# Kernel tuning notes

Hardware: AMD Instinct MI355X
Metric: run time of the kernel (lower is better)

Reference implementation:

```python
import jax, jax.numpy as jnp
import numpy as np

CHEB_K = 3
EMBED_DIM = 16
N_NODES = 2048
DIM = 64


def setup_inputs() -> dict:
    key = jax.random.key(0)
    k1, k2, k3, k4 = jax.random.split(key, 4)
    B, N, T, D = 16, N_NODES, 12, DIM
    x = jax.random.normal(k1, (B, N, T, D), dtype=jnp.float32)
    node_embeddings = jax.random.normal(k2, (N, EMBED_DIM), dtype=jnp.float32)
    # xavier-uniform-ish init for pools
    wp_bound = float(np.sqrt(6.0 / (EMBED_DIM * CHEB_K * D + D)))
    weights_pool = jax.random.uniform(k3, (EMBED_DIM, CHEB_K, D, D), dtype=jnp.float32,
                                      minval=-wp_bound, maxval=wp_bound)
    bias_pool = jax.random.uniform(k4, (EMBED_DIM, D), dtype=jnp.float32)
    return {"x": x, "node_embeddings": node_embeddings,
            "weights_pool": weights_pool, "bias_pool": bias_pool}


def reference(x, node_embeddings, weights_pool, bias_pool):
    B, N, T, D = x.shape
    cheb_k = weights_pool.shape[1]
    # [B,N,T,D] -> [B*T, N, D]
    xr = jnp.transpose(x, (0, 2, 1, 3)).reshape(B * T, N, D)
    # adaptive adjacency: row-softmax of relu gram matrix  [N,N]
    supports = jax.nn.softmax(jax.nn.relu(node_embeddings @ node_embeddings.T), axis=1)
    # Chebyshev polynomial basis of the adaptive support
    support_set = [jnp.eye(N, dtype=supports.dtype), supports]
    for _ in range(2, cheb_k):
        support_set.append(2.0 * supports @ support_set[-1] - support_set[-2])
    supports_k = jnp.stack(support_set, axis=0)  # [K,N,N]
    # hypernetwork: per-node weights/bias from embeddings
    weights = jnp.einsum('nd,dkio->nkio', node_embeddings, weights_pool)  # [N,K,D,D]
    bias = node_embeddings @ bias_pool  # [N,D]
    # graph conv: gather K-hop aggregates, then per-node grouped GEMM
    x_g = jnp.einsum('knm,bmc->bnkc', supports_k, xr)  # [B*T,N,K,D]
    x_gconv = jnp.einsum('bnki,nkio->bno', x_g, weights) + bias  # [B*T,N,D]
    return jnp.transpose(x_gconv.reshape(B, T, N, D), (0, 2, 1, 3))
```

## Files before the change

kernel.cpp:

```cpp
#include <hip/hip_runtime.h>
#include <hip/hip_bf16.h>

#define N_NODES 2048
#define EMB 16
#define NT 12
#define BT 192
#define C_COLS 12288
#define TD 768
#define BSTRIDE (N_NODES * TD)
#define KDIM 2048

typedef unsigned short u16;
typedef unsigned int u32;
typedef __attribute__((ext_vector_type(8))) __bf16 bf16x8;
typedef __attribute__((ext_vector_type(8))) u16 u16x8;
typedef __attribute__((ext_vector_type(4))) float f32x4;

__device__ __forceinline__ u16 f2bfu(float f) {
    u32 u = __float_as_uint(f);
    return (u16)((u + 0x7FFFu + ((u >> 16) & 1u)) >> 16);
}
__device__ __forceinline__ float bfu2f(u16 h) {
    return __uint_as_float(((u32)h) << 16);
}

__device__ __forceinline__ void gl2lds16(const void* g, void* l) {
    __builtin_amdgcn_global_load_lds(
        (const __attribute__((address_space(1))) u32*)g,
        (__attribute__((address_space(3))) u32*)l, 16, 0, 0);
}

__device__ __forceinline__ int cswz(int col, int row) {
    return (col & ~63) | ((((col >> 3) ^ row) & 7) << 3) | (col & 7);
}

__global__ void supports_kernel(const float* __restrict__ E, u16* __restrict__ Sb)
{
    __shared__ float en[EMB];
    __shared__ float red[256];
    const int n = blockIdx.x;
    const int tid = threadIdx.x;
    if (tid < EMB) en[tid] = E[n * EMB + tid];
    __syncthreads();

    float v[8];
    float mx = 0.0f;
    #pragma unroll
    for (int j = 0; j < 8; ++j) {
        const int m = tid + j * 256;
        const float* em = E + m * EMB;
        float acc = 0.f;
        #pragma unroll
        for (int d = 0; d < EMB; ++d) acc += en[d] * em[d];
        acc = fmaxf(acc, 0.f);
        v[j] = acc;
        mx = fmaxf(mx, acc);
    }
    red[tid] = mx;
    __syncthreads();
    for (int s = 128; s > 0; s >>= 1) {
        if (tid < s) red[tid] = fmaxf(red[tid], red[tid + s]);
        __syncthreads();
    }
    mx = red[0];
    __syncthreads();

    float sum = 0.f;
    #pragma unroll
    for (int j = 0; j < 8; ++j) { v[j] = __expf(v[j] - mx); sum += v[j]; }
    red[tid] = sum;
    __syncthreads();
    for (int s = 128; s > 0; s >>= 1) {
        if (tid < s) red[tid] += red[tid + s];
        __syncthreads();
    }
    const float inv = 1.f / red[0];
    #pragma unroll
    for (int j = 0; j < 8; ++j)
        Sb[(size_t)n * KDIM + tid + j * 256] = f2bfu(v[j] * inv);
}

__global__ void supports2_kernel(const float* __restrict__ E, u16* __restrict__ Sb)
{
    __shared__ float en[EMB];
    __shared__ float red[256];
    const int n = blockIdx.x;
    const int tid = threadIdx.x;
    if (tid < EMB) en[tid] = E[n * EMB + tid];
    __syncthreads();

    float v[8];
    float mx = 0.0f;
    #pragma unroll
    for (int j = 0; j < 8; ++j) {
        const int m = tid + j * 256;
        const float* em = E + m * EMB;
        float acc = 0.f;
        #pragma unroll
        for (int d = 0; d < EMB; ++d) acc += en[d] * em[d];
        acc = fmaxf(acc, 0.f);
        v[j] = acc;
        mx = fmaxf(mx, acc);
    }
    red[tid] = mx;
    __syncthreads();
    for (int s = 128; s > 0; s >>= 1) {
        if (tid < s) red[tid] = fmaxf(red[tid], red[tid + s]);
        __syncthreads();
    }
    mx = red[0];
    __syncthreads();

    float sum = 0.f;
    #pragma unroll
    for (int j = 0; j < 8; ++j) { v[j] = __expf(v[j] - mx); sum += v[j]; }
    red[tid] = sum;
    __syncthreads();
    for (int s = 128; s > 0; s >>= 1) {
        if (tid < s) red[tid] += red[tid + s];
        __syncthreads();
    }
    const float inv = 1.f / red[0];
    #pragma unroll
    for (int j = 0; j < 8; ++j) {
        const int m = tid + j * 256;
        Sb[(size_t)n * KDIM + cswz(m, n)] = f2bfu(v[j] * inv);
    }
}

__global__ void strans_kernel(const u16* __restrict__ Sb, u16* __restrict__ SbT)
{
    __shared__ u16 T[64][65];
    const int tid = threadIdx.x;
    const int n0 = blockIdx.y * 64;
    const int j0 = blockIdx.x * 64;
    const int lc = tid & 63;
    const int rg = tid >> 6;
    #pragma unroll
    for (int j = 0; j < 16; ++j) {
        const int r = j * 4 + rg;
        const u16 vv = Sb[(size_t)(n0 + r) * KDIM + j0 + lc];
        const int jt = ((((lc >> 3) ^ (n0 + r)) & 7) << 3) | (lc & 7);
        T[jt][r] = vv;
    }
    __syncthreads();
    #pragma unroll
    for (int j = 0; j < 16; ++j) {
        const int jj = j * 4 + rg;
        const int cs = ((((lc >> 3) ^ (j0 + jj)) & 7) << 3) | (lc & 7);
        SbT[(size_t)(j0 + jj) * KDIM + n0 + cs] = T[jj][lc];
    }
}

__global__ void xcast_kernel(const float* __restrict__ x, u16* __restrict__ XbT, int c0g)
{
    __shared__ u16 tile[64][65];
    const int tid = threadIdx.x;
    const int cg = c0g + blockIdx.x * 64;
    const int b = cg / TD;
    const int r0 = cg - b * TD;
    const int m0 = blockIdx.y * 64;
    const float* xp = x + (size_t)b * BSTRIDE + (size_t)m0 * TD + r0;

    const int lc = tid & 63;
    const int rg = tid >> 6;
    #pragma unroll
    for (int j = 0; j < 16; ++j) {
        const int mr = j * 4 + rg;
        tile[lc][mr] = f2bfu(xp[(size_t)mr * TD + lc]);
    }
    __syncthreads();
    u16* op = XbT + (size_t)(blockIdx.x * 64) * KDIM + m0;
    #pragma unroll
    for (int j = 0; j < 16; ++j) {
        const int cr = j * 4 + rg;
        op[(size_t)cr * KDIM + lc] = tile[cr][lc];
    }
}

__global__ void xcast2_kernel(const float* __restrict__ x, u16* __restrict__ XbT)
{
    __shared__ u16 tile[64][65];
    const int tid = threadIdx.x;
    const int cg = blockIdx.x * 64;
    const int b = cg / TD;
    const int r0 = cg - b * TD;
    const int m0 = blockIdx.y * 64;
    const float* xp = x + (size_t)b * BSTRIDE + (size_t)m0 * TD + r0;

    const int lc = tid & 63;
    const int rg = tid >> 6;
    #pragma unroll
    for (int j = 0; j < 16; ++j) {
        const int mr = j * 4 + rg;
        tile[lc][mr] = f2bfu(xp[(size_t)mr * TD + lc]);
    }
    __syncthreads();
    u16* op = XbT + (size_t)cg * KDIM + m0;
    #pragma unroll
    for (int j = 0; j < 16; ++j) {
        const int cr = j * 4 + rg;
        const int ls = ((((lc >> 3) ^ cr) & 7) << 3) | (lc & 7);
        op[(size_t)cr * KDIM + ls] = tile[cr][lc];
    }
}

template <int MODE>
__launch_bounds__(512, 2)
__global__ void gemm256(const u16* __restrict__ A, const u16* __restrict__ B,
                        u16* __restrict__ O1, u16* __restrict__ O2)
{
    __shared__ char smem[131072];
    const int tid = threadIdx.x;
    const int lane = tid & 63;
    const int w = tid >> 6;
    const int wm = w >> 2, wn = w & 3;
    const int ln15 = lane & 15, quad = lane >> 4;

    const int m0 = blockIdx.y * 256;
    const int c0 = blockIdx.x * 256;

    const int srow = lane >> 3;
    const int sbyte = (lane & 7) * 16;
    const char* gA = (const char*)A + (size_t)(m0 + w * 32 + srow) * 4096 + sbyte;
    const char* gB = (const char*)B + (size_t)(c0 + w * 32 + srow) * 4096 + sbyte;
    char* lA = smem + w * 4096;
    char* lB = smem + 32768 + w * 4096;

    auto stage = [&](int t, int buf) {
        #pragma unroll
        for (int j = 0; j < 4; ++j) {
            gl2lds16(gA + (size_t)j * 32768 + (size_t)t * 128,
                     lA + buf * 65536 + j * 1024);
            gl2lds16(gB + (size_t)j * 32768 + (size_t)t * 128,
                     lB + buf * 65536 + j * 1024);
        }
    };

    stage(0, 0);
    stage(1, 1);
    asm volatile("s_waitcnt vmcnt(8)" ::: "memory");
    __builtin_amdgcn_sched_barrier(0);
    __builtin_amdgcn_s_barrier();

    f32x4 acc[8][4] = {};
    const int arow0 = wm * 128 + ln15;
    const int brow0 = wn * 64 + ln15;
    const int xorm = (ln15 & 7) << 4;

    const int NTI = KDIM / 64;
    #pragma unroll 1
    for (int t = 0; t < NTI; ++t) {
        const char* Ab = smem + (t & 1) * 65536;
        const char* Bb = Ab + 32768;
        #pragma unroll
        for (int kh = 0; kh < 2; ++kh) {
            const int koff = (kh * 64 + quad * 16) ^ xorm;
            bf16x8 af[8], bg[4];
            #pragma unroll
            for (int mi = 0; mi < 8; ++mi)
                af[mi] = *(const bf16x8*)(Ab + (arow0 + mi * 16) * 128 + koff);
            #pragma unroll
            for (int ni = 0; ni < 4; ++ni)
                bg[ni] = *(const bf16x8*)(Bb + (brow0 + ni * 16) * 128 + koff);
            #pragma unroll
            for (int mi = 0; mi < 8; ++mi)
                #pragma unroll
                for (int ni = 0; ni < 4; ++ni)
                    acc[mi][ni] = __builtin_amdgcn_mfma_f32_16x16x32_bf16(
                        af[mi], bg[ni], acc[mi][ni], 0, 0, 0);
        }
        __builtin_amdgcn_sched_barrier(0);
        __builtin_amdgcn_s_barrier();
        __builtin_amdgcn_sched_barrier(0);
        if (t + 2 < NTI) {
            stage(t + 2, t & 1);
            asm volatile("s_waitcnt vmcnt(8)" ::: "memory");
        } else {
            asm volatile("s_waitcnt vmcnt(0)" ::: "memory");
        }
        __builtin_amdgcn_sched_barrier(0);
        __builtin_amdgcn_s_barrier();
        __builtin_amdgcn_sched_barrier(0);
    }

    const int mbase = m0 + wm * 128 + quad * 4;
    const int cbase = c0 + wn * 64 + ln15;
    if (MODE == 0) {
        #pragma unroll
        for (int mi = 0; mi < 8; ++mi) {
            #pragma unroll
            for (int ni = 0; ni < 4; ++ni) {
                const f32x4 v = acc[mi][ni];
                const int cc = cbase + ni * 16;
                #pragma unroll
                for (int r = 0; r < 4; ++r) {
                    const int mm = mbase + mi * 16 + r;
                    const float t2 = 2.f * v[r] - ((mm == cc) ? 1.f : 0.f);
                    O1[(size_t)mm * KDIM + cswz(cc, mm)] = f2bfu(t2);
                }
            }
        }
    } else {
        u16* Ob = (m0 < 2048) ? O1 : O2;
        const int mb = (m0 < 2048) ? mbase : (mbase - 2048);
        #pragma unroll
        for (int mi = 0; mi < 8; ++mi) {
            #pragma unroll
            for (int ni = 0; ni < 4; ++ni) {
                const f32x4 v = acc[mi][ni];
                const int cc = cbase + ni * 16;
                u16* orow = Ob + (size_t)(mb + mi * 16) * C_COLS + cc;
                orow[0 * C_COLS] = f2bfu(v.x);
                orow[1 * C_COLS] = f2bfu(v.y);
                orow[2 * C_COLS] = f2bfu(v.z);
                orow[3 * C_COLS] = f2bfu(v.w);
            }
        }
    }
}

template <int MODE>
__launch_bounds__(256, 3)
__global__ void mfma_gemm(const u16* __restrict__ A,
                          const u16* __restrict__ B,
                          u16* __restrict__ OutT,
                          u16* __restrict__ OutRow,
                          const u16* __restrict__ Xc,
                          int c0g)
{
    __shared__ char smem[16384];
    char* As = smem;
    char* Bs = smem + 8192;

    const int tid = threadIdx.x;
    const int lane = tid & 63;
    const int w = tid >> 6;
    const int wm = w >> 1, wn = w & 1;
    const int ln15 = lane & 15, quad = lane >> 4;

    const int m0 = blockIdx.y * 128;
    const int cb = blockIdx.x * 128;

    const int q0 = 2 * w, q1 = 2 * w + 1;
    const int srow = lane >> 2;
    const int skol = (lane & 3) * 8;
    const u16* ga0 = A + (size_t)(m0 + q0 * 16 + srow) * KDIM + skol;
    const u16* ga1 = A + (size_t)(m0 + q1 * 16 + srow) * KDIM + skol;
    const u16* gb0 = B + (size_t)(cb + q0 * 16 + srow) * KDIM + skol;
    const u16* gb1 = B + (size_t)(cb + q1 * 16 + srow) * KDIM + skol;
    char* la0 = As + q0 * 1024;
    char* la1 = As + q1 * 1024;
    char* lb0 = Bs + q0 * 1024;
    char* lb1 = Bs + q1 * 1024;

    f32x4 acc[4][4] = {};

    for (int k0 = 0; k0 < KDIM; k0 += 32) {
        __syncthreads();
        gl2lds16(ga0, la0);
        gl2lds16(ga1, la1);
        gl2lds16(gb0, lb0);
        gl2lds16(gb1, lb1);
        ga0 += 32; ga1 += 32; gb0 += 32; gb1 += 32;
        __syncthreads();

        bf16x8 af[4], bg[4];
        #pragma unroll
        for (int i = 0; i < 4; ++i) {
            af[i] = *(const bf16x8*)(As + ((wm * 64 + i * 16 + ln15) * 64 + quad * 16));
            bg[i] = *(const bf16x8*)(Bs + ((wn * 64 + i * 16 + ln15) * 64 + quad * 16));
        }
        #pragma unroll
        for (int mi = 0; mi < 4; ++mi)
            #pragma unroll
            for (int ni = 0; ni < 4; ++ni)
                acc[mi][ni] = __builtin_amdgcn_mfma_f32_16x16x32_bf16(
                    af[mi], bg[ni], acc[mi][ni], 0, 0, 0);
    }

    const int mbase = m0 + wm * 64 + quad * 4;
    const int cbase = cb + wn * 64 + ln15;
    #pragma unroll
    for (int mi = 0; mi < 4; ++mi) {
        #pragma unroll
        for (int ni = 0; ni < 4; ++ni) {
            const f32x4 v = acc[mi][ni];
            const int mm = mbase + mi * 16;
            const int cc = cbase + ni * 16;
            if (MODE == 0) {
                ushort4 u;
                u.x = f2bfu(v.x); u.y = f2bfu(v.y); u.z = f2bfu(v.z); u.w = f2bfu(v.w);
                *(ushort4*)(OutT + (size_t)cc * KDIM + mm) = u;
                u16* orow = OutRow + (size_t)mm * C_COLS + c0g + cc;
                orow[0 * C_COLS] = u.x;
                orow[1 * C_COLS] = u.y;
                orow[2 * C_COLS] = u.z;
                orow[3 * C_COLS] = u.w;
            } else {
                const ushort4 xv = *(const ushort4*)(Xc + (size_t)cc * KDIM + mm);
                u16* orow = OutRow + (size_t)mm * C_COLS + c0g + cc;
                orow[0 * C_COLS] = f2bfu(2.f * v.x - bfu2f(xv.x));
                orow[1 * C_COLS] = f2bfu(2.f * v.y - bfu2f(xv.y));
                orow[2 * C_COLS] = f2bfu(2.f * v.z - bfu2f(xv.z));
                orow[3 * C_COLS] = f2bfu(2.f * v.w - bfu2f(xv.w));
            }
        }
    }
}

__launch_bounds__(256, 2)
__global__ void whyper_kernel(const float* __restrict__ E,
                              const float* __restrict__ Wp,
                              u16* __restrict__ Wrow)
{
    __shared__ float Es[32][16];
    const int tid = threadIdx.x;
    const int kt = blockIdx.x;
    const int n0 = blockIdx.y * 32;
    for (int i = tid; i < 512; i += 256)
        Es[i >> 4][i & 15] = E[(n0 + (i >> 4)) * EMB + (i & 15)];
    __syncthreads();

    const int o = tid & 63;
    const int kq = tid >> 6;
    #pragma unroll 1
    for (int it = 0; it < 6; ++it) {
        const int ki = kt * 24 + it * 4 + kq;
        const float* wp = Wp + (size_t)ki * 64 + o;
        float wv[EMB];
        #pragma unroll
        for (int d = 0; d < EMB; ++d) wv[d] = wp[(size_t)d * 12288];
        #pragma unroll 4
        for (int nn = 0; nn < 32; ++nn) {
            float a = 0.f;
            #pragma unroll
            for (int d = 0; d < EMB; ++d) a = fmaf(Es[nn][d], wv[d], a);
            Wrow[(size_t)(n0 + nn) * 12288 + (size_t)ki * 64 + o] = f2bfu(a);
        }
    }
}

__launch_bounds__(256, 2)
__global__ void wtrans_kernel(u16* __restrict__ Wbuf)
{
    __shared__ u16 Wt[64 * 192];
    const int n = blockIdx.x;
    const int tid = threadIdx.x;
    u16* Wn = Wbuf + (size_t)n * 12288;

    ushort4 va[6][2];
    #pragma unroll
    for (int j = 0; j < 6; ++j) {
        const int c = tid + j * 256;
        va[j][0] = *(const ushort4*)(Wn + c * 8);
        va[j][1] = *(const ushort4*)(Wn + c * 8 + 4);
    }
    #pragma unroll
    for (int j = 0; j < 6; ++j) {
        const int c = tid + j * 256;
        const int ki = c >> 3;
        const int o0 = (c & 7) * 8;
        Wt[(o0 + 0) * 192 + ki] = va[j][0].x;
        Wt[(o0 + 1) * 192 + ki] = va[j][0].y;
        Wt[(o0 + 2) * 192 + ki] = va[j][0].z;
        Wt[(o0 + 3) * 192 + ki] = va[j][0].w;
        Wt[(o0 + 4) * 192 + ki] = va[j][1].x;
        Wt[(o0 + 5) * 192 + ki] = va[j][1].y;
        Wt[(o0 + 6) * 192 + ki] = va[j][1].z;
        Wt[(o0 + 7) * 192 + ki] = va[j][1].w;
    }
    __syncthreads();

    #pragma unroll
    for (int j = 0; j < 6; ++j) {
        const int c = tid + j * 256;
        const int o = c / 24;
        const int kc = c - o * 24;
        const int ki0 = kc * 8;
        const int m = (o & 7) << 4;
        const ushort4 lo = *(const ushort4*)(Wt + o * 192 + ki0);
        const ushort4 hi = *(const ushort4*)(Wt + o * 192 + ki0 + 4);
        char* gp = (char*)Wbuf + (size_t)n * 24576 + o * 384 + ((ki0 * 2) ^ m);
        *(ushort4*)gp = lo;
        *(ushort4*)(gp + 8) = hi;
    }
}

__launch_bounds__(256, 4)
__global__ void gconv_mfma2_kernel(const float* __restrict__ x,
                                   const float* __restrict__ E,
                                   const float* __restrict__ Bp,
                                   const u16* __restrict__ Wall,
                                   const u16* __restrict__ Y1,
                                   const u16* __restrict__ Y2,
                                   float* __restrict__ Out)
{
    __shared__ char WsB[24576];
    __shared__ float en[EMB];
    __shared__ float bias[64];

    const int n = blockIdx.x;
    const int tid = threadIdx.x;
    const int lane = tid & 63;
    const int w = tid >> 6;

    if (tid < EMB) en[tid] = E[n * EMB + tid];

    const char* Wn = (const char*)Wall + (size_t)n * 24576;
    for (int iss = w; iss < 24; iss += 4)
        gl2lds16(Wn + iss * 1024 + lane * 16, WsB + iss * 1024);

    __syncthreads();

    if (tid < 64) {
        float a = 0.f;
        #pragma unroll
        for (int d = 0; d < EMB; ++d) a = fmaf(en[d], Bp[d * 64 + tid], a);
        bias[tid] = a;
    }
    __syncthreads();

    const int ln15 = lane & 15, quad = lane >> 4;
    const int q16 = quad * 16;
    const int m0w = w * 48;

    int rowb[4], msk[4];
    #pragma unroll
    for (int ni = 0; ni < 4; ++ni) {
        const int o = ni * 16 + ln15;
        rowb[ni] = o * 384;
        msk[ni] = (o & 7) << 4;
    }

    const float* xb[3];
    size_t yo[3];
    #pragma unroll
    for (int mi = 0; mi < 3; ++mi) {
        const int bt = m0w + mi * 16 + ln15;
        const int b = bt / NT, t = bt - b * NT;
        xb[mi] = x + (size_t)b * BSTRIDE + (size_t)n * TD + (size_t)t * 64 + quad * 8;
        yo[mi] = (size_t)n * C_COLS + (size_t)bt * 64 + quad * 8;
    }

    f32x4 acc[3][4] = {};

    #pragma unroll
    for (int ks = 0; ks < 2; ++ks) {
        bf16x8 af[3];
        #pragma unroll
        for (int mi = 0; mi < 3; ++mi) {
            const float* p = xb[mi] + ks * 32;
            const f32x4 lo = *(const f32x4*)p;
            const f32x4 hi = *(const f32x4*)(p + 4);
            u16x8 u;
            u[0] = f2bfu(lo.x); u[1] = f2bfu(lo.y); u[2] = f2bfu(lo.z); u[3] = f2bfu(lo.w);
            u[4] = f2bfu(hi.x); u[5] = f2bfu(hi.y); u[6] = f2bfu(hi.z); u[7] = f2bfu(hi.w);
            af[mi] = *(const bf16x8*)&u;
        }
        bf16x8 bg[4];
        #pragma unroll
        for (int ni = 0; ni < 4; ++ni)
            bg[ni] = *(const bf16x8*)(WsB + rowb[ni] + ((ks * 64 + q16) ^ msk[ni]));
        #pragma unroll
        for (int mi = 0; mi < 3; ++mi)
            #pragma unroll
            for (int ni = 0; ni < 4; ++ni)
                acc[mi][ni] = __builtin_amdgcn_mfma_f32_16x16x32_bf16(
                    af[mi], bg[ni], acc[mi][ni], 0, 0, 0);
    }

    const u16* ybase[2] = { Y1, Y2 };
    #pragma unroll
    for (int s = 0; s < 2; ++s) {
        const u16* Yb = ybase[s];
        #pragma unroll
        for (int ks = 0; ks < 2; ++ks) {
            bf16x8 af[3];
            #pragma unroll
            for (int mi = 0; mi < 3; ++mi)
                af[mi] = *(const bf16x8*)(Yb + yo[mi] + ks * 32);
            bf16x8 bg[4];
            #pragma unroll
            for (int ni = 0; ni < 4; ++ni)
                bg[ni] = *(const bf16x8*)(WsB + rowb[ni] + 128 + s * 128
                                          + ((ks * 64 + q16) ^ msk[ni]));
            #pragma unroll
            for (int mi = 0; mi < 3; ++mi)
                #pragma unroll
                for (int ni = 0; ni < 4; ++ni)
                    acc[mi][ni] = __builtin_amdgcn_mfma_f32_16x16x32_bf16(
                        af[mi], bg[ni], acc[mi][ni], 0, 0, 0);
        }
    }

    float bv[4];
    #pragma unroll
    for (int ni = 0; ni < 4; ++ni) bv[ni] = bias[ni * 16 + ln15];

    #pragma unroll
    for (int mi = 0; mi < 3; ++mi) {
        const int rowb2 = m0w + mi * 16 + quad * 4;
        #pragma unroll
        for (int r = 0; r < 4; ++r) {
            const int bt = rowb2 + r;
            const int b = bt / NT, t = bt - b * NT;
            float* op = Out + (((size_t)(b * N_NODES + n)) * NT + t) * 64 + ln15;
            #pragma unroll
            for (int ni = 0; ni < 4; ++ni)
                op[ni * 16] = acc[mi][ni][r] + bv[ni];
        }
    }
}

__launch_bounds__(256, 4)
__global__ void gconv_mfma_kernel(const float* __restrict__ x,
                                  const float* __restrict__ E,
                                  const float* __restrict__ Wp,
                                  const float* __restrict__ Bp,
                                  const u16* __restrict__ Y1,
                                  const u16* __restrict__ Y2,
                                  float* __restrict__ Out)
{
    __shared__ u16 Ws[64][200];
    __shared__ float en[EMB];
    __shared__ float bias[64];

    const int n = blockIdx.x;
    const int tid = threadIdx.x;
    if (tid < EMB) en[tid] = E[n * EMB + tid];
    __syncthreads();

    {
        const int o = tid & 63;
        const int kio = tid >> 6;
        #pragma unroll 4
        for (int j = 0; j < 48; ++j) {
            const int ki = j * 4 + kio;
            const float* wp = Wp + ki * 64 + o;
            float a = 0.f;
            #pragma unroll
            for (int d = 0; d < EMB; ++d) a = fmaf(en[d], wp[d * 12288], a);
            Ws[o][ki] = f2bfu(a);
        }
        if (tid < 64) {
            float a = 0.f;
            #pragma unroll
            for (int d = 0; d < EMB; ++d) a = fmaf(en[d], Bp[d * 64 + tid], a);
            bias[tid] = a;
        }
    }
    __syncthreads();

    const int lane = tid & 63;
    const int w = tid >> 6;
    const int ln15 = lane & 15, quad = lane >> 4;
    const int m0w = w * 48;

    const float* xb[3];
    size_t yo[3];
    #pragma unroll
    for (int mi = 0; mi < 3; ++mi) {
        const int bt = m0w + mi * 16 + ln15;
        const int b = bt / NT, t = bt - b * NT;
        xb[mi] = x + (size_t)b * BSTRIDE + (size_t)n * TD + (size_t)t * 64 + quad * 8;
        yo[mi] = (size_t)n * C_COLS + (size_t)bt * 64 + quad * 8;
    }

    f32x4 acc[3][4] = {};

    #pragma unroll
    for (int ks = 0; ks < 2; ++ks) {
        bf16x8 af[3];
        #pragma unroll
        for (int mi = 0; mi < 3; ++mi) {
            const float* p = xb[mi] + ks * 32;
            const f32x4 lo = *(const f32x4*)p;
            const f32x4 hi = *(const f32x4*)(p + 4);
            u16x8 u;
            u[0] = f2bfu(lo.x); u[1] = f2bfu(lo.y); u[2] = f2bfu(lo.z); u[3] = f2bfu(lo.w);
            u[4] = f2bfu(hi.x); u[5] = f2bfu(hi.y); u[6] = f2bfu(hi.z); u[7] = f2bfu(hi.w);
            af[mi] = *(const bf16x8*)&u;
        }
        bf16x8 bg[4];
        #pragma unroll
        for (int ni = 0; ni < 4; ++ni)
            bg[ni] = *(const bf16x8*)&Ws[ni * 16 + ln15][ks * 32 + quad * 8];
        #pragma unroll
        for (int mi = 0; mi < 3; ++mi)
            #pragma unroll
            for (int ni = 0; ni < 4; ++ni)
                acc[mi][ni] = __builtin_amdgcn_mfma_f32_16x16x32_bf16(
                    af[mi], bg[ni], acc[mi][ni], 0, 0, 0);
    }

    const u16* ybase[2] = { Y1, Y2 };
    #pragma unroll
    for (int s = 0; s < 2; ++s) {
        const u16* Yb = ybase[s];
        #pragma unroll
        for (int ks = 0; ks < 2; ++ks) {
            bf16x8 af[3];
            #pragma unroll
            for (int mi = 0; mi < 3; ++mi)
                af[mi] = *(const bf16x8*)(Yb + yo[mi] + ks * 32);
            bf16x8 bg[4];
            #pragma unroll
            for (int ni = 0; ni < 4; ++ni)
                bg[ni] = *(const bf16x8*)&Ws[ni * 16 + ln15][64 + s * 64 + ks * 32 + quad * 8];
            #pragma unroll
            for (int mi = 0; mi < 3; ++mi)
                #pragma unroll
                for (int ni = 0; ni < 4; ++ni)
                    acc[mi][ni] = __builtin_amdgcn_mfma_f32_16x16x32_bf16(
                        af[mi], bg[ni], acc[mi][ni], 0, 0, 0);
        }
    }

    float bv[4];
    #pragma unroll
    for (int ni = 0; ni < 4; ++ni) bv[ni] = bias[ni * 16 + ln15];

    #pragma unroll
    for (int mi = 0; mi < 3; ++mi) {
        const int rowb = m0w + mi * 16 + quad * 4;
        #pragma unroll
        for (int r = 0; r < 4; ++r) {
            const int bt = rowb + r;
            const int b = bt / NT, t = bt - b * NT;
            float* op = Out + (((size_t)(b * N_NODES + n)) * NT + t) * 64 + ln15;
            #pragma unroll
            for (int ni = 0; ni < 4; ++ni)
                op[ni * 16] = acc[mi][ni][r] + bv[ni];
        }
    }
}

extern "C" void kernel_launch(void* const* d_in, const int* in_sizes, int n_in,
                              void* d_out, int out_size, void* d_ws, size_t ws_size,
                              hipStream_t stream)
{
    const float* x  = (const float*)d_in[0];
    const float* E  = (const float*)d_in[1];
    const float* Wp = (const float*)d_in[2];
    const float* Bp = (const float*)d_in[3];
    float* Out = (float*)d_out;

    const size_t MiB = 1024 * 1024;

    if (ws_size >= 216 * MiB) {
        u16* Sb    = (u16*)d_ws;
        u16* T2b   = (u16*)((char*)d_ws + 8 * MiB);
        u16* SbT   = (u16*)((char*)d_ws + 16 * MiB);
        u16* Y1row = (u16*)((char*)d_ws + 24 * MiB);
        u16* Y2row = (u16*)((char*)d_ws + 72 * MiB);
        u16* XbT   = (u16*)((char*)d_ws + 120 * MiB);
        u16* Wbuf  = (u16*)((char*)d_ws + 168 * MiB);

        supports2_kernel<<<N_NODES, 256, 0, stream>>>(E, Sb);
        strans_kernel<<<dim3(32, 32), 256, 0, stream>>>(Sb, SbT);
        gemm256<0><<<dim3(8, 8), 512, 0, stream>>>(Sb, SbT, T2b, nullptr);
        xcast2_kernel<<<dim3(192, 32), 256, 0, stream>>>(x, XbT);
        gemm256<1><<<dim3(48, 16), 512, 0, stream>>>(Sb, XbT, Y1row, Y2row);

        whyper_kernel<<<dim3(8, 64), 256, 0, stream>>>(E, Wp, Wbuf);
        wtrans_kernel<<<N_NODES, 256, 0, stream>>>(Wbuf);
        gconv_mfma2_kernel<<<N_NODES, 256, 0, stream>>>(x, E, Bp, Wbuf, Y1row, Y2row, Out);
        return;
    }

    u16* Sb    = (u16*)d_ws;
    u16* Y1row = (u16*)((char*)d_ws + 8 * MiB);
    u16* Y2row = (u16*)((char*)d_ws + 56 * MiB);
    char* chunkbase = (char*)d_ws + 104 * MiB;

    size_t wall_off = 0;
    bool newpath = false;
    if (ws_size >= 160 * MiB) {
        wall_off = ((ws_size - 48 * MiB) / 256) * 256;
        if (wall_off >= 112 * MiB) newpath = true;
    }
    const size_t budget = newpath ? wall_off : ws_size;

    const int cands[5] = {1, 2, 3, 6, 12};
    int nc = 12;
    for (int i = 0; i < 5; ++i) {
        const size_t chunk_bytes = (size_t)(C_COLS / cands[i]) * KDIM * 2;
        if (104 * MiB + 2 * chunk_bytes <= budget) { nc = cands[i]; break; }
    }
    const int CW = C_COLS / nc;
    u16* XbTc = (u16*)chunkbase;
    u16* Y1Tc = (u16*)(chunkbase + (size_t)CW * KDIM * 2);
    u16* Wbuf = (u16*)((char*)d_ws + wall_off);

    supports_kernel<<<N_NODES, 256, 0, stream>>>(E, Sb);

    if (newpath) {
        whyper_kernel<<<dim3(8, 64), 256, 0, stream>>>(E, Wp, Wbuf);
        wtrans_kernel<<<N_NODES, 256, 0, stream>>>(Wbuf);
    }

    for (int c = 0; c < nc; ++c) {
        const int c0g = c * CW;
        xcast_kernel<<<dim3(CW / 64, 32), 256, 0, stream>>>(x, XbTc, c0g);
        mfma_gemm<0><<<dim3(CW / 128, 16), 256, 0, stream>>>(Sb, XbTc, Y1Tc, Y1row, nullptr, c0g);
        mfma_gemm<1><<<dim3(CW / 128, 16), 256, 0, stream>>>(Sb, Y1Tc, nullptr, Y2row, XbTc, c0g);
    }

    if (newpath)
        gconv_mfma2_kernel<<<N_NODES, 256, 0, stream>>>(x, E, Bp, Wbuf, Y1row, Y2row, Out);
    else
        gconv_mfma_kernel<<<N_NODES, 256, 0, stream>>>(x, E, Wp, Bp, Y1row, Y2row, Out);
}
```

Baseline: 548.0 us.

## Split GEMM inner loop into barrier-synchronized phases with MFMA priority boost

Restructures the bf16 GEMM main loop into four phases per K-tile, each loading a half of the A fragments (and B fragments every other phase), then issuing 16 MFMAs under raised wave priority with s_setprio. Workgroup barriers bracket each phase so waves alternate between LDS-read and MFMA work, aiming to interleave memory and matrix-core activity across waves and cut register pressure from holding 8 A fragments. It adds eight extra barriers per tile, which may cost synchronization overhead.

```diff
diff --git a/kernel.cpp b/kernel.cpp
--- a/kernel.cpp
+++ b/kernel.cpp
@@ -205,6 +205,35 @@
     }
 }
 
+template <int MIH, bool LOADB>
+__device__ __forceinline__ void gphase(const char* Ab, const char* Bb, int koff,
+                                       int arow0, int brow0,
+                                       f32x4 (*acc)[4], bf16x8* bg)
+{
+    if (LOADB) {
+        #pragma unroll
+        for (int ni = 0; ni < 4; ++ni)
+            bg[ni] = *(const bf16x8*)(Bb + (brow0 + ni * 16) * 128 + koff);
+    }
+    bf16x8 af[4];
+    #pragma unroll
+    for (int mi = 0; mi < 4; ++mi)
+        af[mi] = *(const bf16x8*)(Ab + (arow0 + (MIH * 4 + mi) * 16) * 128 + koff);
+    __builtin_amdgcn_s_barrier();
+    asm volatile("s_waitcnt lgkmcnt(0)" ::: "memory");
+    __builtin_amdgcn_sched_barrier(0);
+    __builtin_amdgcn_s_setprio(1);
+    #pragma unroll
+    for (int mi = 0; mi < 4; ++mi)
+        #pragma unroll
+        for (int ni = 0; ni < 4; ++ni)
+            acc[MIH * 4 + mi][ni] = __builtin_amdgcn_mfma_f32_16x16x32_bf16(
+                af[mi], bg[ni], acc[MIH * 4 + mi][ni], 0, 0, 0);
+    __builtin_amdgcn_s_setprio(0);
+    __builtin_amdgcn_sched_barrier(0);
+    __builtin_amdgcn_s_barrier();
+}
+
 template <int MODE>
 __launch_bounds__(512, 2)
 __global__ void gemm256(const u16* __restrict__ A, const u16* __restrict__ B,
@@ -237,51 +266,39 @@
         }
     };
 
+    f32x4 acc[8][4] = {};
+    bf16x8 bg[4];
+    const int arow0 = wm * 128 + ln15;
+    const int brow0 = wn * 64 + ln15;
+    const int xorm = (ln15 & 7) << 4;
+
+    const int NTI = KDIM / 64;
     stage(0, 0);
     stage(1, 1);
     asm volatile("s_waitcnt vmcnt(8)" ::: "memory");
     __builtin_amdgcn_sched_barrier(0);
     __builtin_amdgcn_s_barrier();
 
-    f32x4 acc[8][4] = {};
-    const int arow0 = wm * 128 + ln15;
-    const int brow0 = wn * 64 + ln15;
-    const int xorm = (ln15 & 7) << 4;
-
-    const int NTI = KDIM / 64;
     #pragma unroll 1
     for (int t = 0; t < NTI; ++t) {
-        const char* Ab = smem + (t & 1) * 65536;
+        const int cur = t & 1;
+        const char* Ab = smem + cur * 65536;
         const char* Bb = Ab + 32768;
-        #pragma unroll
-        for (int kh = 0; kh < 2; ++kh) {
-            const int koff = (kh * 64 + quad * 16) ^ xorm;
-            bf16x8 af[8], bg[4];
-            #pragma unroll
-            for (int mi = 0; mi < 8; ++mi)
-                af[mi] = *(const bf16x8*)(Ab + (arow0 + mi * 16) * 128 + koff);
-            #pragma unroll
-            for (int ni = 0; ni < 4; ++ni)
-                bg[ni] = *(const bf16x8*)(Bb + (brow0 + ni * 16) * 128 + koff);
-            #pragma unroll
-            for (int mi = 0; mi < 8; ++mi)
-                #pragma unroll
-                for (int ni = 0; ni < 4; ++ni)
-                    acc[mi][ni] = __builtin_amdgcn_mfma_f32_16x16x32_bf16(
-                        af[mi], bg[ni], acc[mi][ni], 0, 0, 0);
-        }
-        __builtin_amdgcn_sched_barrier(0);
-        __builtin_amdgcn_s_barrier();
-        __builtin_amdgcn_sched_barrier(0);
+        const int k0 = (quad * 16) ^ xorm;
+        const int k1 = (64 + quad * 16) ^ xorm;
+
+        gphase<0, true >(Ab, Bb, k0, arow0, brow0, acc, bg);
+        gphase<1, false>(Ab, Bb, k0, arow0, brow0, acc, bg);
+        gphase<0, true >(Ab, Bb, k1, arow0, brow0, acc, bg);
+        gphase<1, false>(Ab, Bb, k1, arow0, brow0, acc, bg);
         if (t + 2 < NTI) {
-            stage(t + 2, t & 1);
+            stage(t + 2, cur);
             asm volatile("s_waitcnt vmcnt(8)" ::: "memory");
         } else {
             asm volatile("s_waitcnt vmcnt(0)" ::: "memory");
         }
         __builtin_amdgcn_sched_barrier(0);
         __builtin_amdgcn_s_barrier();
-        __builtin_amdgcn_sched_barrier(0);
     }
 
     const int mbase = m0 + wm * 128 + quad * 4;
```

Result: slower. 561.8 us (+2.5%).
